# Kernel tuning notes

Measured on AMD Instinct MI355X. Metric: run time of the kernel, lower is better.

The kernel has to match this reference:

```python
import jax, jax.numpy as jnp
import numpy as np

B, S, D_MODEL, N_HEADS, D_HEAD = 2, 2048, 2048, 16, 128


def _rope_tables(seq_len, d_head, base=10000.0):
    # standard llama RoPE cos/sin tables, broadcastable to (B, H, S, d_head)
    inv_freq = 1.0 / (base ** (np.arange(0, d_head, 2, dtype=np.float32) / d_head))
    t = np.arange(seq_len, dtype=np.float32)
    freqs = np.outer(t, inv_freq)                      # (S, d_head/2)
    emb = np.concatenate([freqs, freqs], axis=-1)       # (S, d_head)
    cos = jnp.asarray(np.cos(emb))[None, None]          # (1,1,S,d_head)
    sin = jnp.asarray(np.sin(emb))[None, None]
    return cos, sin


def setup_inputs() -> dict:
    key = jax.random.key(0)
    ks = jax.random.split(key, 5)
    scale = 0.02
    x = jax.random.normal(ks[0], (B, S, D_MODEL), dtype=jnp.float32)
    Wq = jax.random.normal(ks[1], (D_MODEL, D_MODEL), dtype=jnp.float32) * scale
    Wk = jax.random.normal(ks[2], (D_MODEL, D_MODEL), dtype=jnp.float32) * scale
    Wv = jax.random.normal(ks[3], (D_MODEL, D_MODEL), dtype=jnp.float32) * scale
    Wo = jax.random.normal(ks[4], (D_MODEL, D_MODEL), dtype=jnp.float32) * scale
    cos, sin = _rope_tables(S, D_HEAD)
    return {"x": x, "cos": cos, "sin": sin, "Wq": Wq, "Wk": Wk, "Wv": Wv, "Wo": Wo}


def _rotate_half(x):
    x1, x2 = jnp.split(x, 2, axis=-1)
    return jnp.concatenate([-x2, x1], axis=-1)


def _apply_rope(x, cos, sin):
    return x * cos + _rotate_half(x) * sin


def reference(x, cos, sin, Wq, Wk, Wv, Wo):
    b, s, _ = x.shape
    # QKV projections (nn.Linear computes x @ W.T), reshape to (B, H, S, Dh)
    def proj(W):
        return (x @ W.T).reshape(b, s, N_HEADS, D_HEAD).transpose(0, 2, 1, 3)
    q = _apply_rope(proj(Wq), cos, sin)
    k = _apply_rope(proj(Wk), cos, sin)
    v = proj(Wv)
    # causal scaled dot-product attention
    scale = 1.0 / jnp.sqrt(jnp.asarray(D_HEAD, dtype=x.dtype))
    scores = jnp.einsum("bhqd,bhkd->bhqk", q, k) * scale
    causal = jnp.tril(jnp.ones((s, s), dtype=bool))
    scores = jnp.where(causal, scores, jnp.asarray(-jnp.inf, dtype=scores.dtype))
    attn = jax.nn.softmax(scores, axis=-1)
    vals = jnp.einsum("bhqk,bhkd->bhqd", attn, v)
    vals = vals.transpose(0, 2, 1, 3).reshape(b, s, D_MODEL)
    return vals @ Wo.T
```

## Files before the change

kernel.cpp:

```cpp
#include <hip/hip_runtime.h>

#define S_LEN 2048
#define DMODEL 2048
#define NHEADS 16
#define DHEAD 128
#define BATCH 2

typedef unsigned short u16;
typedef __attribute__((ext_vector_type(8))) __bf16 bf16x8;
typedef __attribute__((ext_vector_type(4))) float f32x4;

__device__ __forceinline__ u16 f2bf(float f) {
    union { float f; unsigned int u; } a; a.f = f;
    unsigned int u = a.u;
    u += 0x7fffu + ((u >> 16) & 1u);
    return (u16)(u >> 16);
}
__device__ __forceinline__ u16 f2bf_fast(float f) {
    union { float f; unsigned int u; } a; a.f = f;
    return (u16)((a.u + 0x8000u) >> 16);
}
__device__ __forceinline__ float bf2f(u16 b) {
    union { unsigned int u; float f; } a; a.u = ((unsigned int)b) << 16;
    return a.f;
}

__device__ __forceinline__ void g2l16(const void* g, void* l) {
    __builtin_amdgcn_global_load_lds((const __attribute__((address_space(1))) unsigned int*)g,
                                     (__attribute__((address_space(3))) unsigned int*)l,
                                     16, 0, 0);
}

__global__ void cvt_bf16(const float* __restrict__ in, u16* __restrict__ out, int n4) {
    int i = blockIdx.x * 256 + threadIdx.x;
    if (i >= n4) return;
    f32x4 v = *(const f32x4*)(in + (size_t)i * 4);
    ushort4 o;
    o.x = f2bf(v[0]); o.y = f2bf(v[1]); o.z = f2bf(v[2]); o.w = f2bf(v[3]);
    *(ushort4*)(out + (size_t)i * 4) = o;
}

__global__ void cvt_w4(const float* __restrict__ w0, const float* __restrict__ w1,
                       const float* __restrict__ w2, const float* __restrict__ w3,
                       u16* __restrict__ dst, int n4) {
    int y = blockIdx.y;
    const float* src = (y == 0) ? w0 : (y == 1) ? w1 : (y == 2) ? w2 : w3;
    u16* out = dst + (size_t)y * DMODEL * DMODEL;
    int i = blockIdx.x * 256 + threadIdx.x;
    if (i >= n4) return;
    f32x4 v = *(const f32x4*)(src + (size_t)i * 4);
    ushort4 o;
    o.x = f2bf(v[0]); o.y = f2bf(v[1]); o.z = f2bf(v[2]); o.w = f2bf(v[3]);
    *(ushort4*)(out + (size_t)i * 4) = o;
}

#define QK_PRESCALE 0.12751744f
__global__ void rope_kernel(u16* __restrict__ Q, u16* __restrict__ K,
                            const float* __restrict__ cosT, const float* __restrict__ sinT) {
    u16* T = blockIdx.z ? K : Q;
    const float pre = blockIdx.z ? 1.0f : QK_PRESCALE;
    int bh = blockIdx.y;
    int t = blockIdx.x * 256 + threadIdx.x;
    int s = t >> 6;
    int d = t & 63;
    u16* row = T + ((size_t)bh * S_LEN + s) * DHEAD;
    float c  = cosT[s * DHEAD + d];
    float sn = sinT[s * DHEAD + d];
    float q1 = bf2f(row[d]);
    float q2 = bf2f(row[d + 64]);
    row[d]      = f2bf((q1 * c - q2 * sn) * pre);
    row[d + 64] = f2bf((q2 * c + q1 * sn) * pre);
}

__global__ __launch_bounds__(256) void gemm_qkv(const u16* __restrict__ A,
                                                const u16* __restrict__ W,
                                                u16* __restrict__ Qo,
                                                u16* __restrict__ Ko,
                                                u16* __restrict__ Vto) {
    __shared__ u16 As[128 * 32];
    __shared__ u16 Ws[128 * 32];
    const int tid  = threadIdx.x;
    const int lane = tid & 63;
    const int wave = tid >> 6;
    const int wm = wave >> 1, wn = wave & 1;
    const int col = lane & 15, quad = lane >> 4;
    const int m0 = blockIdx.y * 128, n0 = blockIdx.x * 128;
    const int K = DMODEL;

    f32x4 acc[4][4] = {};

    for (int kk = 0; kk < K; kk += 32) {
        #pragma unroll
        for (int i = 0; i < 2; ++i) {
            int c = i * 256 + tid;
            int row = c >> 2, ko = (c & 3) * 8;
            int cb = i * 256 + wave * 64;
            g2l16(A + (size_t)(m0 + row) * K + kk + ko, (void*)(As + cb * 8));
            g2l16(W + (size_t)(n0 + row) * K + kk + ko, (void*)(Ws + cb * 8));
        }
        __syncthreads();
        bf16x8 af[4], wf[4];
        #pragma unroll
        for (int mi = 0; mi < 4; ++mi)
            af[mi] = *(const bf16x8*)&As[(wm * 64 + mi * 16 + col) * 32 + quad * 8];
        #pragma unroll
        for (int ni = 0; ni < 4; ++ni)
            wf[ni] = *(const bf16x8*)&Ws[(wn * 64 + ni * 16 + col) * 32 + quad * 8];
        #pragma unroll
        for (int mi = 0; mi < 4; ++mi)
            #pragma unroll
            for (int ni = 0; ni < 4; ++ni)
                acc[mi][ni] = __builtin_amdgcn_mfma_f32_16x16x32_bf16(af[mi], wf[ni], acc[mi][ni], 0, 0, 0);
        __syncthreads();
    }

    const int which = n0 >> 11;
    if (which == 2) {
        #pragma unroll
        for (int mi = 0; mi < 4; ++mi) {
            #pragma unroll
            for (int ni = 0; ni < 4; ++ni) {
                int s0   = m0 + wm * 64 + mi * 16 + quad * 4;
                int ncol = (n0 & 2047) + wn * 64 + ni * 16 + col;
                int b = s0 >> 11, s = s0 & 2047;
                int h = ncol >> 7, d = ncol & 127;
                ushort4 o;
                o.x = f2bf(acc[mi][ni][0]); o.y = f2bf(acc[mi][ni][1]);
                o.z = f2bf(acc[mi][ni][2]); o.w = f2bf(acc[mi][ni][3]);
                *(ushort4*)&Vto[(((size_t)(b * NHEADS + h)) * DHEAD + d) * S_LEN + s] = o;
            }
        }
    } else {
        u16* out = which ? Ko : Qo;
        #pragma unroll
        for (int mi = 0; mi < 4; ++mi)
            #pragma unroll
            for (int ni = 0; ni < 4; ++ni)
                #pragma unroll
                for (int r = 0; r < 4; ++r) {
                    int row  = m0 + wm * 64 + mi * 16 + quad * 4 + r;
                    int ncol = (n0 & 2047) + wn * 64 + ni * 16 + col;
                    int b = row >> 11, s = row & 2047;
                    int h = ncol >> 7, d = ncol & 127;
                    out[(((size_t)(b * NHEADS + h)) * S_LEN + s) * DHEAD + d] = f2bf(acc[mi][ni][r]);
                }
    }
}

__global__ __launch_bounds__(256) void gemm_out(const u16* __restrict__ A,
                                                const u16* __restrict__ W,
                                                float* __restrict__ out) {
    __shared__ u16 As[128 * 32];
    __shared__ u16 Ws[128 * 32];
    const int tid  = threadIdx.x;
    const int lane = tid & 63;
    const int wave = tid >> 6;
    const int wm = wave >> 1, wn = wave & 1;
    const int col = lane & 15, quad = lane >> 4;
    const int m0 = blockIdx.y * 128, n0 = blockIdx.x * 128;
    const int K = DMODEL;

    f32x4 acc[4][4] = {};

    for (int kk = 0; kk < K; kk += 32) {
        #pragma unroll
        for (int i = 0; i < 2; ++i) {
            int c = i * 256 + tid;
            int row = c >> 2, ko = (c & 3) * 8;
            int cb = i * 256 + wave * 64;
            g2l16(A + (size_t)(m0 + row) * K + kk + ko, (void*)(As + cb * 8));
            g2l16(W + (size_t)(n0 + row) * K + kk + ko, (void*)(Ws + cb * 8));
        }
        __syncthreads();
        bf16x8 af[4], wf[4];
        #pragma unroll
        for (int mi = 0; mi < 4; ++mi)
            af[mi] = *(const bf16x8*)&As[(wm * 64 + mi * 16 + col) * 32 + quad * 8];
        #pragma unroll
        for (int ni = 0; ni < 4; ++ni)
            wf[ni] = *(const bf16x8*)&Ws[(wn * 64 + ni * 16 + col) * 32 + quad * 8];
        #pragma unroll
        for (int mi = 0; mi < 4; ++mi)
            #pragma unroll
            for (int ni = 0; ni < 4; ++ni)
                acc[mi][ni] = __builtin_amdgcn_mfma_f32_16x16x32_bf16(af[mi], wf[ni], acc[mi][ni], 0, 0, 0);
        __syncthreads();
    }

    #pragma unroll
    for (int mi = 0; mi < 4; ++mi)
        #pragma unroll
        for (int ni = 0; ni < 4; ++ni)
            #pragma unroll
            for (int r = 0; r < 4; ++r) {
                int row  = m0 + wm * 64 + mi * 16 + quad * 4 + r;
                int ncol = n0 + wn * 64 + ni * 16 + col;
                out[(size_t)row * DMODEL + ncol] = acc[mi][ni][r];
            }
}

__global__ __launch_bounds__(256) void attn_kernel(const u16* __restrict__ Q,
                                                   const u16* __restrict__ K,
                                                   const u16* __restrict__ Vt,
                                                   u16* __restrict__ Ao) {
    __shared__ u16 Ks[32 * 136];
    __shared__ u16 Vs[128 * 40];
    __shared__ u16 Ps[4][16 * 40];

    const int tid  = threadIdx.x;
    const int lane = tid & 63;
    const int wave = tid >> 6;
    const int col = lane & 15, quad = lane >> 4;
    const int xcd = blockIdx.x & 7;
    const int sub = (blockIdx.x >> 3) & 3;
    const int bh  = xcd * 4 + sub;
    const int qtile = 31 - (int)(blockIdx.x >> 5);
    const int b = bh >> 4, h = bh & 15;
    const int qb = qtile * 64;
    const int qw = qb + wave * 16;

    const u16* Qb = Q  + (size_t)bh * S_LEN * DHEAD;
    const u16* Kb = K  + (size_t)bh * S_LEN * DHEAD;
    const u16* Vb = Vt + (size_t)bh * DHEAD * S_LEN;

    bf16x8 qf[4];
    #pragma unroll
    for (int dc = 0; dc < 4; ++dc)
        qf[dc] = *(const bf16x8*)&Qb[(size_t)(qw + col) * DHEAD + dc * 32 + quad * 8];

    f32x4 accO[8] = {};
    float mrow = -1e30f, lrow = 0.0f;

    const int kend = qb + 64;
    for (int kb = 0; kb < kend; kb += 32) {
        #pragma unroll
        for (int i = 0; i < 2; ++i) {
            int c = tid + i * 256;
            int kr = c >> 4, ko = (c & 15) * 8;
            *(f32x4*)&Ks[kr * 136 + ko] = *(const f32x4*)&Kb[(size_t)(kb + kr) * DHEAD + ko];
            int vr = c >> 2, vo = (c & 3) * 8;
            *(f32x4*)&Vs[vr * 40 + vo] = *(const f32x4*)&Vb[(size_t)vr * S_LEN + kb + vo];
        }
        __syncthreads();

        if (kb <= qw + 15) {
            f32x4 sc[2] = {};
            #pragma unroll
            for (int t = 0; t < 2; ++t)
                #pragma unroll
                for (int dc = 0; dc < 4; ++dc) {
                    bf16x8 kf = *(const bf16x8*)&Ks[(t * 16 + col) * 136 + dc * 32 + quad * 8];
                    sc[t] = __builtin_amdgcn_mfma_f32_16x16x32_bf16(kf, qf[dc], sc[t], 0, 0, 0);
                }

            const int q_g = qw + col;
            float sv[2][4];
            #pragma unroll
            for (int t = 0; t < 2; ++t)
                #pragma unroll
                for (int r = 0; r < 4; ++r) {
                    int k_g = kb + t * 16 + quad * 4 + r;
                    sv[t][r] = (k_g <= q_g) ? sc[t][r] : -1e30f;
                }

            float m01 = fmaxf(fmaxf(sv[0][0], sv[0][1]), fmaxf(sv[0][2], sv[0][3]));
            float m23 = fmaxf(fmaxf(sv[1][0], sv[1][1]), fmaxf(sv[1][2], sv[1][3]));
            float mloc = fmaxf(m01, m23);
            mloc = fmaxf(mloc, __shfl_xor(mloc, 16));
            mloc = fmaxf(mloc, __shfl_xor(mloc, 32));
            float mn = fmaxf(mrow, mloc);
            float al = exp2f(mrow - mn);

            float p[2][4], rloc = 0.0f;
            #pragma unroll
            for (int t = 0; t < 2; ++t)
                #pragma unroll
                for (int r = 0; r < 4; ++r) {
                    p[t][r] = exp2f(sv[t][r] - mn);
                    rloc += p[t][r];
                }
            rloc += __shfl_xor(rloc, 16);
            rloc += __shfl_xor(rloc, 32);
            lrow = lrow * al + rloc;
            mrow = mn;

            if (__any(al != 1.0f)) {
                float alb[4];
                #pragma unroll
                for (int r = 0; r < 4; ++r)
                    alb[r] = __shfl(al, quad * 4 + r);
                #pragma unroll
                for (int ni = 0; ni < 8; ++ni)
                    #pragma unroll
                    for (int r = 0; r < 4; ++r)
                        accO[ni][r] *= alb[r];
            }

            u16* P = Ps[wave];
            #pragma unroll
            for (int t = 0; t < 2; ++t) {
                ushort4 o;
                o.x = f2bf_fast(p[t][0]); o.y = f2bf_fast(p[t][1]);
                o.z = f2bf_fast(p[t][2]); o.w = f2bf_fast(p[t][3]);
                *(ushort4*)&P[col * 40 + t * 16 + quad * 4] = o;
            }
            asm volatile("s_waitcnt lgkmcnt(0)" ::: "memory");
            bf16x8 pf = *(const bf16x8*)&P[col * 40 + quad * 8];

            #pragma unroll
            for (int ni = 0; ni < 8; ++ni) {
                bf16x8 vf = *(const bf16x8*)&Vs[(ni * 16 + col) * 40 + quad * 8];
                accO[ni] = __builtin_amdgcn_mfma_f32_16x16x32_bf16(pf, vf, accO[ni], 0, 0, 0);
            }
        }
        __syncthreads();
    }

    float lb[4];
    #pragma unroll
    for (int r = 0; r < 4; ++r)
        lb[r] = 1.0f / __shfl(lrow, quad * 4 + r);
    #pragma unroll
    for (int ni = 0; ni < 8; ++ni)
        #pragma unroll
        for (int r = 0; r < 4; ++r) {
            int q_g = qw + quad * 4 + r;
            int d = ni * 16 + col;
            Ao[((size_t)(b * S_LEN + q_g)) * DMODEL + h * DHEAD + d] = f2bf(accO[ni][r] * lb[r]);
        }
}

extern "C" void kernel_launch(void* const* d_in, const int* in_sizes, int n_in,
                              void* d_out, int out_size, void* d_ws, size_t ws_size,
                              hipStream_t stream) {
    const float* x    = (const float*)d_in[0];
    const float* cosT = (const float*)d_in[1];
    const float* sinT = (const float*)d_in[2];
    const float* Wq   = (const float*)d_in[3];
    const float* Wk   = (const float*)d_in[4];
    const float* Wv   = (const float*)d_in[5];
    const float* Wo   = (const float*)d_in[6];

    char* ws = (char*)d_ws;
    size_t off = 0;
    auto carve = [&](size_t bytes) {
        void* p = ws + off;
        off += (bytes + 255) & ~(size_t)255;
        return p;
    };
    const size_t xN = (size_t)BATCH * S_LEN * DMODEL;
    const size_t wN = (size_t)DMODEL * DMODEL;
    u16* xb   = (u16*)carve(xN * 2);
    u16* wqkv = (u16*)carve(wN * 2 * 4);
    u16* wob  = wqkv + wN * 3;
    u16* Qb   = (u16*)carve(xN * 2);
    u16* Kb   = (u16*)carve(xN * 2);
    u16* Vtb  = (u16*)carve(xN * 2);
    u16* attn = xb;

    cvt_bf16<<<(int)(xN / 4 / 256), 256, 0, stream>>>(x, xb, (int)(xN / 4));
    cvt_w4<<<dim3((int)(wN / 4 / 256), 4), 256, 0, stream>>>(Wq, Wk, Wv, Wo, wqkv, (int)(wN / 4));

    gemm_qkv<<<dim3(48, 32), 256, 0, stream>>>(xb, wqkv, Qb, Kb, Vtb);

    rope_kernel<<<dim3(S_LEN * 64 / 256, BATCH * NHEADS, 2), 256, 0, stream>>>(Qb, Kb, cosT, sinT);

    attn_kernel<<<dim3(1024), 256, 0, stream>>>(Qb, Kb, Vtb, attn);

    gemm_out<<<dim3(16, 32), 256, 0, stream>>>(attn, wob, (float*)d_out);
}
```

Before: 441.9 us.

## XOR-swizzle LDS tiles and remap GEMM blocks across XCDs

Replaces padded LDS layouts in the GEMMs and attention kernel with XOR-swizzled layouts, so fragment reads avoid bank conflicts without padding. The GEMM grids become 1D and are remapped so that blocks on the same XCD share N-columns of the weight matrix, which should improve L2 reuse. The risk is that the swizzle patterns for the async global-to-LDS writes and the ds_read offsets must match exactly. A mismatch would corrupt results, and any remaining conflicts would limit the benefit.

```diff
diff --git a/kernel.cpp b/kernel.cpp
--- a/kernel.cpp
+++ b/kernel.cpp
@@ -84,16 +84,29 @@
     const int wave = tid >> 6;
     const int wm = wave >> 1, wn = wave & 1;
     const int col = lane & 15, quad = lane >> 4;
-    const int m0 = blockIdx.y * 128, n0 = blockIdx.x * 128;
+    const int blk = blockIdx.x;
+    const int xcd = blk & 7;
+    const int loc = blk >> 3;
+    const int nb  = xcd * 6 + loc % 6;
+    const int mb  = loc / 6;
+    const int m0 = mb * 128, n0 = nb * 128;
     const int K = DMODEL;
 
     f32x4 acc[4][4] = {};
+
+    const int swl = (quad ^ ((col >> 1) & 3)) * 8;
+    int a_off[4], w_off[4];
+    #pragma unroll
+    for (int mi = 0; mi < 4; ++mi) a_off[mi] = (wm * 64 + mi * 16 + col) * 32 + swl;
+    #pragma unroll
+    for (int ni = 0; ni < 4; ++ni) w_off[ni] = (wn * 64 + ni * 16 + col) * 32 + swl;
 
     for (int kk = 0; kk < K; kk += 32) {
         #pragma unroll
         for (int i = 0; i < 2; ++i) {
             int c = i * 256 + tid;
-            int row = c >> 2, ko = (c & 3) * 8;
+            int row = c >> 2;
+            int ko = (((c & 3) ^ ((c >> 3) & 3))) * 8;
             int cb = i * 256 + wave * 64;
             g2l16(A + (size_t)(m0 + row) * K + kk + ko, (void*)(As + cb * 8));
             g2l16(W + (size_t)(n0 + row) * K + kk + ko, (void*)(Ws + cb * 8));
@@ -101,11 +114,9 @@
         __syncthreads();
         bf16x8 af[4], wf[4];
         #pragma unroll
-        for (int mi = 0; mi < 4; ++mi)
-            af[mi] = *(const bf16x8*)&As[(wm * 64 + mi * 16 + col) * 32 + quad * 8];
-        #pragma unroll
-        for (int ni = 0; ni < 4; ++ni)
-            wf[ni] = *(const bf16x8*)&Ws[(wn * 64 + ni * 16 + col) * 32 + quad * 8];
+        for (int mi = 0; mi < 4; ++mi) af[mi] = *(const bf16x8*)&As[a_off[mi]];
+        #pragma unroll
+        for (int ni = 0; ni < 4; ++ni) wf[ni] = *(const bf16x8*)&Ws[w_off[ni]];
         #pragma unroll
         for (int mi = 0; mi < 4; ++mi)
             #pragma unroll
@@ -157,16 +168,29 @@
     const int wave = tid >> 6;
     const int wm = wave >> 1, wn = wave & 1;
     const int col = lane & 15, quad = lane >> 4;
-    const int m0 = blockIdx.y * 128, n0 = blockIdx.x * 128;
+    const int blk = blockIdx.x;
+    const int xcd = blk & 7;
+    const int loc = blk >> 3;
+    const int nb  = xcd * 2 + (loc & 1);
+    const int mb  = loc >> 1;
+    const int m0 = mb * 128, n0 = nb * 128;
     const int K = DMODEL;
 
     f32x4 acc[4][4] = {};
+
+    const int swl = (quad ^ ((col >> 1) & 3)) * 8;
+    int a_off[4], w_off[4];
+    #pragma unroll
+    for (int mi = 0; mi < 4; ++mi) a_off[mi] = (wm * 64 + mi * 16 + col) * 32 + swl;
+    #pragma unroll
+    for (int ni = 0; ni < 4; ++ni) w_off[ni] = (wn * 64 + ni * 16 + col) * 32 + swl;
 
     for (int kk = 0; kk < K; kk += 32) {
         #pragma unroll
         for (int i = 0; i < 2; ++i) {
             int c = i * 256 + tid;
-            int row = c >> 2, ko = (c & 3) * 8;
+            int row = c >> 2;
+            int ko = (((c & 3) ^ ((c >> 3) & 3))) * 8;
             int cb = i * 256 + wave * 64;
             g2l16(A + (size_t)(m0 + row) * K + kk + ko, (void*)(As + cb * 8));
             g2l16(W + (size_t)(n0 + row) * K + kk + ko, (void*)(Ws + cb * 8));
@@ -174,11 +198,9 @@
         __syncthreads();
         bf16x8 af[4], wf[4];
         #pragma unroll
-        for (int mi = 0; mi < 4; ++mi)
-            af[mi] = *(const bf16x8*)&As[(wm * 64 + mi * 16 + col) * 32 + quad * 8];
-        #pragma unroll
-        for (int ni = 0; ni < 4; ++ni)
-            wf[ni] = *(const bf16x8*)&Ws[(wn * 64 + ni * 16 + col) * 32 + quad * 8];
+        for (int mi = 0; mi < 4; ++mi) af[mi] = *(const bf16x8*)&As[a_off[mi]];
+        #pragma unroll
+        for (int ni = 0; ni < 4; ++ni) wf[ni] = *(const bf16x8*)&Ws[w_off[ni]];
         #pragma unroll
         for (int mi = 0; mi < 4; ++mi)
             #pragma unroll
@@ -203,9 +225,9 @@
                                                    const u16* __restrict__ K,
                                                    const u16* __restrict__ Vt,
                                                    u16* __restrict__ Ao) {
-    __shared__ u16 Ks[32 * 136];
-    __shared__ u16 Vs[128 * 40];
-    __shared__ u16 Ps[4][16 * 40];
+    __shared__ u16 Ks[32 * 128];
+    __shared__ u16 Vs[128 * 32];
+    __shared__ u16 Ps[4][16 * 32];
 
     const int tid  = threadIdx.x;
     const int lane = tid & 63;
@@ -228,6 +250,14 @@
     for (int dc = 0; dc < 4; ++dc)
         qf[dc] = *(const bf16x8*)&Qb[(size_t)(qw + col) * DHEAD + dc * 32 + quad * 8];
 
+    const int swl = (quad ^ ((col >> 1) & 3)) * 8;
+    int koff[2][4];
+    #pragma unroll
+    for (int t = 0; t < 2; ++t)
+        #pragma unroll
+        for (int dc = 0; dc < 4; ++dc)
+            koff[t][dc] = (t * 16 + col) * 128 + (((dc * 4 + quad) ^ (col & 7)) * 8);
+
     f32x4 accO[8] = {};
     float mrow = -1e30f, lrow = 0.0f;
 
@@ -236,10 +266,12 @@
         #pragma unroll
         for (int i = 0; i < 2; ++i) {
             int c = tid + i * 256;
-            int kr = c >> 4, ko = (c & 15) * 8;
-            *(f32x4*)&Ks[kr * 136 + ko] = *(const f32x4*)&Kb[(size_t)(kb + kr) * DHEAD + ko];
-            int vr = c >> 2, vo = (c & 3) * 8;
-            *(f32x4*)&Vs[vr * 40 + vo] = *(const f32x4*)&Vb[(size_t)vr * S_LEN + kb + vo];
+            int kr = c >> 4, ko = c & 15;
+            *(f32x4*)&Ks[kr * 128 + ((ko ^ (kr & 7)) * 8)] =
+                *(const f32x4*)&Kb[(size_t)(kb + kr) * DHEAD + ko * 8];
+            int vr = c >> 2, vc = c & 3;
+            *(f32x4*)&Vs[vr * 32 + (((vc ^ ((c >> 3) & 3))) * 8)] =
+                *(const f32x4*)&Vb[(size_t)vr * S_LEN + kb + vc * 8];
         }
         __syncthreads();
 
@@ -249,7 +281,7 @@
             for (int t = 0; t < 2; ++t)
                 #pragma unroll
                 for (int dc = 0; dc < 4; ++dc) {
-                    bf16x8 kf = *(const bf16x8*)&Ks[(t * 16 + col) * 136 + dc * 32 + quad * 8];
+                    bf16x8 kf = *(const bf16x8*)&Ks[koff[t][dc]];
                     sc[t] = __builtin_amdgcn_mfma_f32_16x16x32_bf16(kf, qf[dc], sc[t], 0, 0, 0);
                 }
 
@@ -302,14 +334,15 @@
                 ushort4 o;
                 o.x = f2bf_fast(p[t][0]); o.y = f2bf_fast(p[t][1]);
                 o.z = f2bf_fast(p[t][2]); o.w = f2bf_fast(p[t][3]);
-                *(ushort4*)&P[col * 40 + t * 16 + quad * 4] = o;
+                int chunk = t * 2 + (quad >> 1);
+                *(ushort4*)&P[col * 32 + ((chunk ^ ((col >> 1) & 3)) * 8) + (quad & 1) * 4] = o;
             }
             asm volatile("s_waitcnt lgkmcnt(0)" ::: "memory");
-            bf16x8 pf = *(const bf16x8*)&P[col * 40 + quad * 8];
+            bf16x8 pf = *(const bf16x8*)&P[col * 32 + swl];
 
             #pragma unroll
             for (int ni = 0; ni < 8; ++ni) {
-                bf16x8 vf = *(const bf16x8*)&Vs[(ni * 16 + col) * 40 + quad * 8];
+                bf16x8 vf = *(const bf16x8*)&Vs[(ni * 16 + col) * 32 + swl];
                 accO[ni] = __builtin_amdgcn_mfma_f32_16x16x32_bf16(pf, vf, accO[ni], 0, 0, 0);
             }
         }
@@ -361,11 +394,11 @@
     cvt_bf16<<<(int)(xN / 4 / 256), 256, 0, stream>>>(x, xb, (int)(xN / 4));
     cvt_w4<<<dim3((int)(wN / 4 / 256), 4), 256, 0, stream>>>(Wq, Wk, Wv, Wo, wqkv, (int)(wN / 4));
 
-    gemm_qkv<<<dim3(48, 32), 256, 0, stream>>>(xb, wqkv, Qb, Kb, Vtb);
+    gemm_qkv<<<dim3(1536), 256, 0, stream>>>(xb, wqkv, Qb, Kb, Vtb);
 
     rope_kernel<<<dim3(S_LEN * 64 / 256, BATCH * NHEADS, 2), 256, 0, stream>>>(Qb, Kb, cosT, sinT);
 
     attn_kernel<<<dim3(1024), 256, 0, stream>>>(Qb, Kb, Vtb, attn);
 
-    gemm_out<<<dim3(16, 32), 256, 0, stream>>>(attn, wob, (float*)d_out);
-}
+    gemm_out<<<dim3(512), 256, 0, stream>>>(attn, wob, (float*)d_out);
+}
```

New measurement: 460.7 us. +4.3%, slower.
